# Kernel optimization log

Measured on AMD Instinct MI355X. Metric: run time of the kernel, lower is better.

## Reference

```python
import jax, jax.numpy as jnp
import numpy as np

DECAY = 0.999
EPS = 1e-05
COMMITMENT_COST = 0.25
M, D = 1024, 256
B, H, W = 32, 32, 32


def setup_inputs() -> dict:
    key = jax.random.key(0)
    k1, k2 = jax.random.split(key)
    init_bound = 1.0 / M
    x = jax.random.normal(k1, (B, H, W, D), dtype=jnp.float32)
    embedding = jax.random.uniform(k2, (M, D), dtype=jnp.float32,
                                   minval=-init_bound, maxval=init_bound)
    ema_count = jnp.zeros((M,), dtype=jnp.float32)
    ema_weight = embedding  # buffer initialized as embedding.clone()
    return {"x": x, "embedding": embedding, "ema_count": ema_count,
            "ema_weight": ema_weight}


def reference(x, embedding, ema_count, ema_weight):
    Mn, Dn = embedding.shape
    x_flat = jax.lax.stop_gradient(x).reshape(-1, Dn)          # [N, D]
    N = x_flat.shape[0]

    # (-cdist)^2 == squared euclidean distance; argmin is the same.
    x_sq = jnp.sum(x_flat * x_flat, axis=-1, keepdims=True)    # [N, 1]
    e_sq = jnp.sum(embedding * embedding, axis=-1)             # [M]
    distances = x_sq - 2.0 * (x_flat @ embedding.T) + e_sq[None, :]  # [N, M]
    indices = jnp.argmin(distances, axis=-1)                   # [N]

    quantized = embedding[indices].reshape(x.shape)            # gather

    # one-hot column sums == scatter-add of ones; encodings.T @ x_flat == scatter-add rows
    counts = jnp.zeros((Mn,), x.dtype).at[indices].add(1.0)    # [M]
    dw = jnp.zeros((Mn, Dn), x.dtype).at[indices].add(x_flat)  # [M, D]

    new_count = DECAY * ema_count + (1.0 - DECAY) * counts
    n = jnp.sum(new_count)
    new_count = (new_count + EPS) / (n + Mn * EPS) * n
    new_weight = DECAY * ema_weight + (1.0 - DECAY) * dw
    new_embedding = new_weight / new_count[:, None]

    codebook_loss = jnp.mean((jax.lax.stop_gradient(x) - quantized) ** 2)
    e_latent_loss = jnp.mean((x - jax.lax.stop_gradient(quantized)) ** 2)
    commitment_loss = COMMITMENT_COST * e_latent_loss

    quantized_st = x + jax.lax.stop_gradient(quantized - x)    # straight-through

    avg_probs = counts / N
    perplexity = jnp.exp(-jnp.sum(avg_probs * jnp.log(avg_probs + 1e-10)))

    return (quantized_st, commitment_loss, codebook_loss, perplexity,
            new_embedding, new_count, new_weight)
```

## Files before the change

### kernel.cpp

```cpp
#include <hip/hip_runtime.h>
#include <cfloat>
#include <math.h>

#define N_TOK 32768
#define DIM   256
#define MCODE 1024

typedef unsigned short u16;
typedef unsigned long long u64;
typedef __attribute__((ext_vector_type(8))) short short8;
typedef __attribute__((ext_vector_type(4))) float f32x4;

constexpr float DECAY_ = 0.999f;
constexpr float OMD_   = (float)(1.0 - 0.999);
constexpr float EPS_   = 1e-5f;
constexpr float MEPS_  = (float)(1024 * 1e-5);

constexpr int WS_EH     = 0;
constexpr int WS_EL     = 131072;
constexpr int WS_ESQ    = 262144;
constexpr int WS_CNTI   = 263168;
constexpr int WS_START  = 264192;
constexpr int WS_CURSOR = 265216;
constexpr int WS_BI     = 266240;
constexpr int WS_ROWL   = 299008;
constexpr int WS_LP     = 331776;
constexpr int WS_KEY    = 333824;

constexpr int OUT_Q        = 0;
constexpr int OUT_COMMIT   = 8388608;
constexpr int OUT_CODEBOOK = 8388609;
constexpr int OUT_PERP     = 8388610;
constexpr int OUT_NE       = 8388611;
constexpr int OUT_NC       = 8650755;
constexpr int OUT_NW       = 8651779;

static __device__ __forceinline__ u16 f2bf(float f) {
    unsigned u = __float_as_uint(f);
    unsigned r = (u + 0x7fff + ((u >> 16) & 1)) >> 16;
    return (u16)r;
}
static __device__ __forceinline__ float bf2f(u16 h) {
    return __uint_as_float(((unsigned)h) << 16);
}
static __device__ __forceinline__ void gl2lds16(const u16* g, char* l) {
    __builtin_amdgcn_global_load_lds(
        (const __attribute__((address_space(1))) unsigned int*)g,
        (__attribute__((address_space(3))) unsigned int*)l, 16, 0, 0);
}
static __device__ __forceinline__ unsigned fmap(float f) {
    unsigned u = __float_as_uint(f);
    return (u & 0x80000000u) ? ~u : (u | 0x80000000u);
}

static __device__ __forceinline__ void pack_wave(const float* __restrict__ src,
                                                 u16* __restrict__ dh,
                                                 u16* __restrict__ dl,
                                                 int wave_id, int lane) {
    int rb = wave_id >> 6, kc = (wave_id >> 3) & 7, t = wave_id & 7;
    int row = rb * 128 + t * 16 + (lane & 15);
    int k   = kc * 32 + (lane >> 4) * 8;
    const float* s = &src[row * DIM + k];
    float4 v0 = *(const float4*)s, v1 = *(const float4*)(s + 4);
    float vv[8] = {v0.x, v0.y, v0.z, v0.w, v1.x, v1.y, v1.z, v1.w};
    short8 hv, lv;
#pragma unroll
    for (int j = 0; j < 8; ++j) {
        float v = vv[j];
        u16 h = f2bf(v);
        float r = v - bf2f(h);
        hv[j] = (short)h;
        lv[j] = (short)f2bf(r);
    }
    size_t o = (size_t)wave_id * 512 + lane * 8;
    *(short8*)&dh[o] = hv;
    *(short8*)&dl[o] = lv;
}

__global__ __launch_bounds__(256) void vq_prep(const float* __restrict__ emb,
                                               u16* __restrict__ eh,
                                               u16* __restrict__ el,
                                               float* __restrict__ esq,
                                               u64* __restrict__ keys,
                                               int* __restrict__ cnti) {
    const int b = blockIdx.x, tid = threadIdx.x;
    const int lane = tid & 63, w = tid >> 6;
    if (b < 128) {
        pack_wave(emb, eh, el, b * 4 + w, lane);
    } else if (b < 384) {
        int c = (b - 128) * 4 + w;
        float4 v = *(const float4*)&emb[c * DIM + lane * 4];
        float s = v.x * v.x + v.y * v.y + v.z * v.z + v.w * v.w;
#pragma unroll
        for (int off = 32; off; off >>= 1) s += __shfl_xor(s, off, 64);
        if (lane == 0) esq[c] = s;
    } else if (b < 512) {
        keys[(b - 384) * 256 + tid] = ~0ULL;
    } else {
#pragma unroll
        for (int i = 0; i < 4; ++i) cnti[i * 256 + tid] = 0;
    }
}

__global__ __launch_bounds__(256) void vq_pack_x(const float* __restrict__ x,
                                                 u16* __restrict__ xh,
                                                 u16* __restrict__ xl) {
    int gtid = blockIdx.x * 256 + threadIdx.x;
    pack_wave(x, xh, xl, gtid >> 6, gtid & 63);
}

__global__ __launch_bounds__(256) void vq_scores_mfma(const u16* __restrict__ xh,
                                                      const u16* __restrict__ xl,
                                                      const u16* __restrict__ eh,
                                                      const u16* __restrict__ el,
                                                      const float* __restrict__ esq,
                                                      u64* __restrict__ keys) {
    __shared__ __align__(16) char smem[33792];
    const int tid  = threadIdx.x;
    const int lane = tid & 63, w = tid >> 6;
    const int wm = w & 1, wn = w >> 1;
    const int raw = blockIdx.x;
    const int rb = (raw >> 6) * 8 + (raw & 7);
    const int cs = (raw >> 3) & 7;

    const u16* gb[4] = {xh + (size_t)rb * 32768, xl + (size_t)rb * 32768,
                        eh + (size_t)cs * 32768, el + (size_t)cs * 32768};

    const short8* Ah = (const short8*)(smem);
    const short8* Al = (const short8*)(smem + 8192);
    const short8* Bh = (const short8*)(smem + 16384);
    const short8* Bl = (const short8*)(smem + 24576);

    f32x4 acc[4][4];
#pragma unroll
    for (int i = 0; i < 4; ++i)
#pragma unroll
        for (int j = 0; j < 4; ++j) acc[i][j] = (f32x4)0.f;

    for (int kc = 0; kc < 8; ++kc) {
        __syncthreads();
        {
            const u16* g = gb[w] + kc * 4096 + lane * 8;
            char* l = smem + w * 8192;
#pragma unroll
            for (int s2 = 0; s2 < 8; ++s2)
                gl2lds16(g + s2 * 512, l + s2 * 1024);
        }
        __syncthreads();

        short8 ah[4], al[4];
#pragma unroll
        for (int tm = 0; tm < 4; ++tm) {
            int idx = (wm * 4 + tm) * 64 + lane;
            ah[tm] = Ah[idx];
            al[tm] = Al[idx];
        }
#pragma unroll
        for (int tn = 0; tn < 4; ++tn) {
            int bidx = (wn * 4 + tn) * 64 + lane;
            short8 bh = Bh[bidx], bl = Bl[bidx];
#pragma unroll
            for (int tm = 0; tm < 4; ++tm) {
                acc[tm][tn] = __builtin_amdgcn_mfma_f32_16x16x32_bf16(ah[tm], bh, acc[tm][tn], 0, 0, 0);
                acc[tm][tn] = __builtin_amdgcn_mfma_f32_16x16x32_bf16(al[tm], bh, acc[tm][tn], 0, 0, 0);
                acc[tm][tn] = __builtin_amdgcn_mfma_f32_16x16x32_bf16(ah[tm], bl, acc[tm][tn], 0, 0, 0);
            }
        }
    }

    __syncthreads();
    float* cv = (float*)smem;
    int*   ci = (int*)(smem + 16896);
    const int ln = lane & 15, quad = lane >> 4;
#pragma unroll
    for (int tm = 0; tm < 4; ++tm) {
        float bv[4];
        int   bi[4];
#pragma unroll
        for (int r = 0; r < 4; ++r) { bv[r] = FLT_MAX; bi[r] = 0; }
#pragma unroll
        for (int tn = 0; tn < 4; ++tn) {
            int c = cs * 128 + wn * 64 + tn * 16 + ln;
            float ec = esq[c];
#pragma unroll
            for (int r = 0; r < 4; ++r) {
                float d = fmaf(-2.f, acc[tm][tn][r], ec);
                if (d < bv[r]) { bv[r] = d; bi[r] = c; }
            }
        }
        int row0 = wm * 64 + tm * 16 + quad * 4;
        int slot = wn * 16 + ln;
#pragma unroll
        for (int r = 0; r < 4; ++r) {
            cv[(row0 + r) * 33 + slot] = bv[r];
            ci[(row0 + r) * 33 + slot] = bi[r];
        }
    }
    __syncthreads();
    if (tid < 128) {
        float bv = cv[tid * 33];
        int   bi = ci[tid * 33];
#pragma unroll
        for (int s = 1; s < 32; ++s) {
            float v = cv[tid * 33 + s];
            int  ix = ci[tid * 33 + s];
            if (v < bv || (v == bv && ix < bi)) { bv = v; bi = ix; }
        }
        u64 key = ((u64)fmap(bv) << 32) | (unsigned)bi;
        atomicMin(&keys[rb * 128 + tid], key);
    }
}

__global__ __launch_bounds__(256) void vq_quant(const float* __restrict__ x,
                                                const float* __restrict__ emb,
                                                const u64* __restrict__ keys,
                                                float* __restrict__ outq,
                                                int* __restrict__ cnti,
                                                int* __restrict__ bi_arr,
                                                float* __restrict__ lpart) {
    const int tid = threadIdx.x, lane = tid & 63, w = tid >> 6;
    const float4* x4 = (const float4*)x;
    const float4* e4 = (const float4*)emb;
    float4* o4 = (float4*)outq;
    float lacc = 0.f;
#pragma unroll
    for (int it = 0; it < 4; ++it) {
        int row = blockIdx.x * 16 + it * 4 + w;
        int bi = (int)(unsigned)(keys[row] & 0xffffffffULL);
        if (lane == 0) { atomicAdd(&cnti[bi], 1); bi_arr[row] = bi; }
        float4 xv = x4[row * 64 + lane];
        float4 ev = e4[bi * 64 + lane];
        float4 q;
        q.x = xv.x + (ev.x - xv.x);  q.y = xv.y + (ev.y - xv.y);
        q.z = xv.z + (ev.z - xv.z);  q.w = xv.w + (ev.w - xv.w);
        o4[row * 64 + lane] = q;
        float dx = xv.x - ev.x, dy = xv.y - ev.y, dz = xv.z - ev.z, dwv = xv.w - ev.w;
        lacc += dx * dx + dy * dy + dz * dz + dwv * dwv;
    }
#pragma unroll
    for (int off = 32; off; off >>= 1) lacc += __shfl_xor(lacc, off, 64);
    __shared__ float red[4];
    if (lane == 0) red[w] = lacc;
    __syncthreads();
    if (tid == 0) lpart[blockIdx.x] = red[0] + red[1] + red[2] + red[3];
}

__global__ __launch_bounds__(1024) void vq_scan(const int* __restrict__ cnti,
                                                int* __restrict__ start,
                                                int* __restrict__ cursor) {
    const int m = threadIdx.x;
    __shared__ int s[1024];
    int v = cnti[m];
    s[m] = v;
    __syncthreads();
    for (int off = 1; off < 1024; off <<= 1) {
        int t = (m >= off) ? s[m - off] : 0;
        __syncthreads();
        s[m] += t;
        __syncthreads();
    }
    int excl = s[m] - v;
    start[m] = excl;
    cursor[m] = excl;
}

__global__ __launch_bounds__(256) void vq_fill(const int* __restrict__ bi_arr,
                                               int* __restrict__ cursor,
                                               int* __restrict__ rowlist) {
    int row = blockIdx.x * 256 + threadIdx.x;
    int bi = bi_arr[row];
    int slot = atomicAdd(&cursor[bi], 1);
    rowlist[slot] = row;
}

__global__ __launch_bounds__(1024) void vq_finalize(const int* __restrict__ cnti,
                                                    const float* __restrict__ ema_count,
                                                    const float* __restrict__ lpart,
                                                    float* __restrict__ out) {
    const int m = threadIdx.x;
    __shared__ float red[1024];
    float c   = (float)cnti[m];
    float raw = DECAY_ * ema_count[m] + OMD_ * c;
    red[m] = raw;
    __syncthreads();
    for (int s = 512; s; s >>= 1) { if (m < s) red[m] += red[m + s]; __syncthreads(); }
    float n = red[0];
    __syncthreads();
    out[OUT_NC + m] = (raw + EPS_) / (n + MEPS_) * n;

    float p = c / (float)N_TOK;
    red[m] = p * logf(p + 1e-10f);
    __syncthreads();
    for (int s = 512; s; s >>= 1) { if (m < s) red[m] += red[m + s]; __syncthreads(); }
    float ent = red[0];
    __syncthreads();

    red[m] = lpart[m] + lpart[m + 1024];
    __syncthreads();
    for (int s = 512; s; s >>= 1) { if (m < s) red[m] += red[m + s]; __syncthreads(); }
    if (m == 0) {
        float mean = red[0] / (float)(N_TOK * DIM);
        out[OUT_COMMIT]   = 0.25f * mean;
        out[OUT_CODEBOOK] = mean;
        out[OUT_PERP]     = expf(-ent);
    }
}

__global__ __launch_bounds__(256) void vq_wsum(const float* __restrict__ x,
                                               const int* __restrict__ rowlist,
                                               const int* __restrict__ start,
                                               const int* __restrict__ cnti,
                                               const float* __restrict__ ema_weight,
                                               float* __restrict__ out) {
    const int m = blockIdx.x, d = threadIdx.x;
    int s0 = start[m], n = cnti[m], e = s0 + n;
    float a0 = 0.f, a1 = 0.f, a2 = 0.f, a3 = 0.f;
    int i = s0;
    for (; i + 4 <= e; i += 4) {
        int r0 = rowlist[i], r1 = rowlist[i + 1];
        int r2 = rowlist[i + 2], r3 = rowlist[i + 3];
        a0 += x[r0 * DIM + d];
        a1 += x[r1 * DIM + d];
        a2 += x[r2 * DIM + d];
        a3 += x[r3 * DIM + d];
    }
    for (; i < e; ++i) a0 += x[rowlist[i] * DIM + d];
    float dwsum = (a0 + a1) + (a2 + a3);
    float nw = DECAY_ * ema_weight[m * DIM + d] + OMD_ * dwsum;
    float nc = out[OUT_NC + m];
    out[OUT_NW + m * DIM + d] = nw;
    out[OUT_NE + m * DIM + d] = nw / nc;
}

extern "C" void kernel_launch(void* const* d_in, const int* in_sizes, int n_in,
                              void* d_out, int out_size, void* d_ws, size_t ws_size,
                              hipStream_t stream) {
    const float* x          = (const float*)d_in[0];
    const float* emb        = (const float*)d_in[1];
    const float* ema_count  = (const float*)d_in[2];
    const float* ema_weight = (const float*)d_in[3];
    float* out = (float*)d_out;
    float* wf  = (float*)d_ws;

    u16* xh = (u16*)d_out;
    u16* xl = xh + (size_t)N_TOK * DIM;
    u16* eh = (u16*)(wf + WS_EH);
    u16* el = (u16*)(wf + WS_EL);

    float* esq    = wf + WS_ESQ;
    int*   cnti   = (int*)(wf + WS_CNTI);
    int*   start  = (int*)(wf + WS_START);
    int*   cursor = (int*)(wf + WS_CURSOR);
    int*   bi_arr = (int*)(wf + WS_BI);
    int*   rowl   = (int*)(wf + WS_ROWL);
    float* lpart  = wf + WS_LP;
    u64*   keys   = (u64*)(wf + WS_KEY);

    vq_prep<<<513, 256, 0, stream>>>(emb, eh, el, esq, keys, cnti);
    vq_pack_x<<<4096, 256, 0, stream>>>(x, xh, xl);
    vq_scores_mfma<<<2048, 256, 0, stream>>>(xh, xl, eh, el, esq, keys);
    vq_quant<<<2048, 256, 0, stream>>>(x, emb, keys, out, cnti, bi_arr, lpart);
    vq_scan<<<1, 1024, 0, stream>>>(cnti, start, cursor);
    vq_fill<<<128, 256, 0, stream>>>(bi_arr, cursor, rowl);
    vq_finalize<<<1, 1024, 0, stream>>>(cnti, ema_count, lpart, out);
    vq_wsum<<<MCODE, 256, 0, stream>>>(x, rowl, start, cnti, ema_weight, out);
}
```

Baseline: 186.3 us.

## Fuse prep kernels and replace scan/fill/finalize/wsum with one per-code kernel

Merges the embedding prep and x packing into a single launch, and replaces the scan, fill, finalize and weight-sum kernels with one kernel that has one block per code. Each block scans the full index array to build its own row list in shared memory and recomputes the global count sum redundantly. This removes four launches and the serialized single-block scan and finalize, but makes every block read all 32768 indices (1024x redundant reads of bi_arr), with a slow fallback path for codes whose count exceeds the shared-memory cap.

```diff
diff --git a/kernel.cpp b/kernel.cpp
--- a/kernel.cpp
+++ b/kernel.cpp
@@ -16,16 +16,13 @@
 constexpr float EPS_   = 1e-5f;
 constexpr float MEPS_  = (float)(1024 * 1e-5);
 
-constexpr int WS_EH     = 0;
-constexpr int WS_EL     = 131072;
-constexpr int WS_ESQ    = 262144;
-constexpr int WS_CNTI   = 263168;
-constexpr int WS_START  = 264192;
-constexpr int WS_CURSOR = 265216;
-constexpr int WS_BI     = 266240;
-constexpr int WS_ROWL   = 299008;
-constexpr int WS_LP     = 331776;
-constexpr int WS_KEY    = 333824;
+constexpr int WS_EH   = 0;
+constexpr int WS_EL   = 131072;
+constexpr int WS_ESQ  = 262144;
+constexpr int WS_CNTI = 263168;
+constexpr int WS_BI   = 264192;
+constexpr int WS_LP   = 296960;
+constexpr int WS_KEY  = 299008;
 
 constexpr int OUT_Q        = 0;
 constexpr int OUT_COMMIT   = 8388608;
@@ -77,36 +74,34 @@
     *(short8*)&dl[o] = lv;
 }
 
-__global__ __launch_bounds__(256) void vq_prep(const float* __restrict__ emb,
-                                               u16* __restrict__ eh,
-                                               u16* __restrict__ el,
-                                               float* __restrict__ esq,
-                                               u64* __restrict__ keys,
-                                               int* __restrict__ cnti) {
+__global__ __launch_bounds__(256) void vq_setup(const float* __restrict__ x,
+                                                const float* __restrict__ emb,
+                                                u16* __restrict__ xh,
+                                                u16* __restrict__ xl,
+                                                u16* __restrict__ eh,
+                                                u16* __restrict__ el,
+                                                float* __restrict__ esq,
+                                                u64* __restrict__ keys,
+                                                int* __restrict__ cnti) {
     const int b = blockIdx.x, tid = threadIdx.x;
     const int lane = tid & 63, w = tid >> 6;
-    if (b < 128) {
-        pack_wave(emb, eh, el, b * 4 + w, lane);
-    } else if (b < 384) {
-        int c = (b - 128) * 4 + w;
+    if (b < 4096) { pack_wave(x, xh, xl, b * 4 + w, lane); return; }
+    const int p = b - 4096;
+    if (p < 128) {
+        pack_wave(emb, eh, el, p * 4 + w, lane);
+    } else if (p < 384) {
+        int c = (p - 128) * 4 + w;
         float4 v = *(const float4*)&emb[c * DIM + lane * 4];
         float s = v.x * v.x + v.y * v.y + v.z * v.z + v.w * v.w;
 #pragma unroll
         for (int off = 32; off; off >>= 1) s += __shfl_xor(s, off, 64);
         if (lane == 0) esq[c] = s;
-    } else if (b < 512) {
-        keys[(b - 384) * 256 + tid] = ~0ULL;
+    } else if (p < 512) {
+        keys[(p - 384) * 256 + tid] = ~0ULL;
     } else {
 #pragma unroll
         for (int i = 0; i < 4; ++i) cnti[i * 256 + tid] = 0;
     }
-}
-
-__global__ __launch_bounds__(256) void vq_pack_x(const float* __restrict__ x,
-                                                 u16* __restrict__ xh,
-                                                 u16* __restrict__ xl) {
-    int gtid = blockIdx.x * 256 + threadIdx.x;
-    pack_wave(x, xh, xl, gtid >> 6, gtid & 63);
 }
 
 __global__ __launch_bounds__(256) void vq_scores_mfma(const u16* __restrict__ xh,
@@ -245,91 +240,94 @@
     if (tid == 0) lpart[blockIdx.x] = red[0] + red[1] + red[2] + red[3];
 }
 
-__global__ __launch_bounds__(1024) void vq_scan(const int* __restrict__ cnti,
-                                                int* __restrict__ start,
-                                                int* __restrict__ cursor) {
-    const int m = threadIdx.x;
-    __shared__ int s[1024];
-    int v = cnti[m];
-    s[m] = v;
-    __syncthreads();
-    for (int off = 1; off < 1024; off <<= 1) {
-        int t = (m >= off) ? s[m - off] : 0;
-        __syncthreads();
-        s[m] += t;
-        __syncthreads();
-    }
-    int excl = s[m] - v;
-    start[m] = excl;
-    cursor[m] = excl;
-}
-
-__global__ __launch_bounds__(256) void vq_fill(const int* __restrict__ bi_arr,
-                                               int* __restrict__ cursor,
-                                               int* __restrict__ rowlist) {
-    int row = blockIdx.x * 256 + threadIdx.x;
-    int bi = bi_arr[row];
-    int slot = atomicAdd(&cursor[bi], 1);
-    rowlist[slot] = row;
-}
-
-__global__ __launch_bounds__(1024) void vq_finalize(const int* __restrict__ cnti,
-                                                    const float* __restrict__ ema_count,
-                                                    const float* __restrict__ lpart,
-                                                    float* __restrict__ out) {
-    const int m = threadIdx.x;
-    __shared__ float red[1024];
-    float c   = (float)cnti[m];
-    float raw = DECAY_ * ema_count[m] + OMD_ * c;
-    red[m] = raw;
-    __syncthreads();
-    for (int s = 512; s; s >>= 1) { if (m < s) red[m] += red[m + s]; __syncthreads(); }
-    float n = red[0];
-    __syncthreads();
-    out[OUT_NC + m] = (raw + EPS_) / (n + MEPS_) * n;
-
-    float p = c / (float)N_TOK;
-    red[m] = p * logf(p + 1e-10f);
-    __syncthreads();
-    for (int s = 512; s; s >>= 1) { if (m < s) red[m] += red[m + s]; __syncthreads(); }
-    float ent = red[0];
-    __syncthreads();
-
-    red[m] = lpart[m] + lpart[m + 1024];
-    __syncthreads();
-    for (int s = 512; s; s >>= 1) { if (m < s) red[m] += red[m + s]; __syncthreads(); }
+#define MEGA_CAP 6144
+__global__ __launch_bounds__(256) void vq_mega(const float* __restrict__ x,
+                                               const float* __restrict__ ema_count,
+                                               const float* __restrict__ ema_weight,
+                                               const int* __restrict__ cnti,
+                                               const int* __restrict__ bi_arr,
+                                               const float* __restrict__ lpart,
+                                               float* __restrict__ out) {
+    const int m = blockIdx.x, tid = threadIdx.x;
+    __shared__ float fs[256];
+    __shared__ int list[MEGA_CAP];
+    __shared__ int lcount;
+
+    float rsum = 0.f;
+#pragma unroll
+    for (int i = 0; i < 4; ++i) {
+        int mm = tid * 4 + i;
+        rsum += DECAY_ * ema_count[mm] + OMD_ * (float)cnti[mm];
+    }
+    fs[tid] = rsum;
+    if (tid == 0) lcount = 0;
+    __syncthreads();
+    for (int s = 128; s; s >>= 1) { if (tid < s) fs[tid] += fs[tid + s]; __syncthreads(); }
+    const float n = fs[0];
+    __syncthreads();
+
+    const int nm = cnti[m];
+    float dwsum;
+    if (nm <= MEGA_CAP) {
+        for (int i = tid; i < N_TOK; i += 256)
+            if (bi_arr[i] == m) { int p = atomicAdd(&lcount, 1); list[p] = i; }
+        __syncthreads();
+        float a0 = 0.f, a1 = 0.f, a2 = 0.f, a3 = 0.f;
+        int i = 0;
+        for (; i + 4 <= nm; i += 4) {
+            a0 += x[list[i]     * DIM + tid];
+            a1 += x[list[i + 1] * DIM + tid];
+            a2 += x[list[i + 2] * DIM + tid];
+            a3 += x[list[i + 3] * DIM + tid];
+        }
+        for (; i < nm; ++i) a0 += x[list[i] * DIM + tid];
+        dwsum = (a0 + a1) + (a2 + a3);
+    } else {
+        __shared__ int chunk[256];
+        float a0 = 0.f;
+        for (int base = 0; base < N_TOK; base += 256) {
+            __syncthreads();
+            chunk[tid] = bi_arr[base + tid];
+            __syncthreads();
+            for (int j = 0; j < 256; ++j)
+                if (chunk[j] == m) a0 += x[(base + j) * DIM + tid];
+        }
+        dwsum = a0;
+    }
+
+    float raw_m = DECAY_ * ema_count[m] + OMD_ * (float)nm;
+    float ncm = (raw_m + EPS_) / (n + MEPS_) * n;
+    float nw = DECAY_ * ema_weight[m * DIM + tid] + OMD_ * dwsum;
+    out[OUT_NW + m * DIM + tid] = nw;
+    out[OUT_NE + m * DIM + tid] = nw / ncm;
+    if (tid == 0) out[OUT_NC + m] = ncm;
+
     if (m == 0) {
-        float mean = red[0] / (float)(N_TOK * DIM);
-        out[OUT_COMMIT]   = 0.25f * mean;
-        out[OUT_CODEBOOK] = mean;
-        out[OUT_PERP]     = expf(-ent);
-    }
-}
-
-__global__ __launch_bounds__(256) void vq_wsum(const float* __restrict__ x,
-                                               const int* __restrict__ rowlist,
-                                               const int* __restrict__ start,
-                                               const int* __restrict__ cnti,
-                                               const float* __restrict__ ema_weight,
-                                               float* __restrict__ out) {
-    const int m = blockIdx.x, d = threadIdx.x;
-    int s0 = start[m], n = cnti[m], e = s0 + n;
-    float a0 = 0.f, a1 = 0.f, a2 = 0.f, a3 = 0.f;
-    int i = s0;
-    for (; i + 4 <= e; i += 4) {
-        int r0 = rowlist[i], r1 = rowlist[i + 1];
-        int r2 = rowlist[i + 2], r3 = rowlist[i + 3];
-        a0 += x[r0 * DIM + d];
-        a1 += x[r1 * DIM + d];
-        a2 += x[r2 * DIM + d];
-        a3 += x[r3 * DIM + d];
-    }
-    for (; i < e; ++i) a0 += x[rowlist[i] * DIM + d];
-    float dwsum = (a0 + a1) + (a2 + a3);
-    float nw = DECAY_ * ema_weight[m * DIM + d] + OMD_ * dwsum;
-    float nc = out[OUT_NC + m];
-    out[OUT_NW + m * DIM + d] = nw;
-    out[OUT_NE + m * DIM + d] = nw / nc;
+        float ent = 0.f;
+#pragma unroll
+        for (int i = 0; i < 4; ++i) {
+            float p = (float)cnti[tid * 4 + i] / (float)N_TOK;
+            ent += p * logf(p + 1e-10f);
+        }
+        __syncthreads();
+        fs[tid] = ent;
+        __syncthreads();
+        for (int s = 128; s; s >>= 1) { if (tid < s) fs[tid] += fs[tid + s]; __syncthreads(); }
+        float entr = fs[0];
+        __syncthreads();
+        float ls = 0.f;
+#pragma unroll
+        for (int k = 0; k < 8; ++k) ls += lpart[tid + 256 * k];
+        fs[tid] = ls;
+        __syncthreads();
+        for (int s = 128; s; s >>= 1) { if (tid < s) fs[tid] += fs[tid + s]; __syncthreads(); }
+        if (tid == 0) {
+            float mean = fs[0] / (float)(N_TOK * DIM);
+            out[OUT_COMMIT]   = 0.25f * mean;
+            out[OUT_CODEBOOK] = mean;
+            out[OUT_PERP]     = expf(-entr);
+        }
+    }
 }
 
 extern "C" void kernel_launch(void* const* d_in, const int* in_sizes, int n_in,
@@ -349,19 +347,13 @@
 
     float* esq    = wf + WS_ESQ;
     int*   cnti   = (int*)(wf + WS_CNTI);
-    int*   start  = (int*)(wf + WS_START);
-    int*   cursor = (int*)(wf + WS_CURSOR);
     int*   bi_arr = (int*)(wf + WS_BI);
-    int*   rowl   = (int*)(wf + WS_ROWL);
     float* lpart  = wf + WS_LP;
     u64*   keys   = (u64*)(wf + WS_KEY);
 
-    vq_prep<<<513, 256, 0, stream>>>(emb, eh, el, esq, keys, cnti);
-    vq_pack_x<<<4096, 256, 0, stream>>>(x, xh, xl);
+    vq_setup<<<4609, 256, 0, stream>>>(x, emb, xh, xl, eh, el, esq, keys, cnti);
     vq_scores_mfma<<<2048, 256, 0, stream>>>(xh, xl, eh, el, esq, keys);
     vq_quant<<<2048, 256, 0, stream>>>(x, emb, keys, out, cnti, bi_arr, lpart);
-    vq_scan<<<1, 1024, 0, stream>>>(cnti, start, cursor);
-    vq_fill<<<128, 256, 0, stream>>>(bi_arr, cursor, rowl);
-    vq_finalize<<<1, 1024, 0, stream>>>(cnti, ema_count, lpart, out);
-    vq_wsum<<<MCODE, 256, 0, stream>>>(x, rowl, start, cnti, ema_weight, out);
-}
+    vq_mega<<<MCODE, 256, 0, stream>>>(x, ema_count, ema_weight, cnti, bi_arr,
+                                       lpart, out);
+}
```

New measurement: 198.5 us. 1.07x slower.
